# Optimization experiments

Measured on AMD Instinct MI355X. Metric: run time of the kernel, lower is better.

Reference implementation:

```python
import jax, jax.numpy as jnp
import numpy as np

K = 128      # knowledge_n (= net1 = prednet output width)
LOW = 64     # low_dim
PP = 64      # pp_dim
STU = 50000  # student_n
EXER = 20000 # exer_n
S_RANGES = [(0, 9999), (10000, 19999)]
NR = len(S_RANGES)
B = 4096


def setup_inputs() -> dict:
    key = jax.random.key(0)
    ks = jax.random.split(key, 16)

    def xavier(k, shape):
        fan_in, fan_out = shape[-1], shape[-2] if len(shape) > 1 else shape[-1]
        lim = np.sqrt(6.0 / (fan_in + fan_out))
        return jax.random.uniform(k, shape, jnp.float32, -lim, lim)

    return {
        "stu_id": jax.random.randint(ks[0], (B,), 0, STU),
        "exer_id": jax.random.randint(ks[1], (B,), 0, EXER),
        "kn_emb": jnp.ones((B, K), jnp.float32),
        "student_emb": xavier(ks[2], (NR, STU, LOW)),          # ParameterList stacked
        "prompt_stu": xavier(ks[3], (STU, PP)),
        "knowledge_emb": jax.random.normal(ks[4], (K, LOW), jnp.float32),
        "k_difficulty": xavier(ks[5], (EXER, LOW)),
        "s_exer_vectors": jax.random.uniform(ks[6], (NR, PP), jnp.float32),
        "W1": xavier(ks[7], (K, K + LOW)),                      # prednet_full1 (no bias)
        "W2": xavier(ks[8], (K, K + LOW)),                      # prednet_full2 (no bias)
        "W3": xavier(ks[9], (1, K)),                            # prednet_full3
        "b3": jnp.zeros((1,), jnp.float32),
        "fc1_W": xavier(ks[10], (K, PP + K)),
        "fc1_b": jnp.zeros((K,), jnp.float32),
        "fc2_W": xavier(ks[11], (K, PP + K)),
        "fc2_b": jnp.zeros((K,), jnp.float32),
    }


def reference(stu_id, exer_id, kn_emb, student_emb, prompt_stu, knowledge_emb,
              k_difficulty, s_exer_vectors, W1, W2, W3, b3, fc1_W, fc1_b, fc2_W, fc2_b):
    sig = jax.nn.sigmoid
    kle = knowledge_emb  # [K, LOW]

    # --- student side ---
    # prompt_stu.repeat(NR, 1) then index_select == index prompt_stu with stu_id % STU
    p_stu = prompt_stu[stu_id % STU]                              # [B, PP]
    stu_cat = student_emb.reshape(NR * STU, LOW)                  # concat of ParameterList
    old_stu = sig(stu_cat[stu_id] @ kle.T)                        # [B, K]
    stu_e = sig(jnp.concatenate([p_stu, old_stu], 1) @ fc1_W.T + fc1_b)  # [B, K]

    # --- exercise side ---
    counts = np.array([r[1] - r[0] + 1 for r in S_RANGES])
    temp_vectors = jnp.repeat(s_exer_vectors, counts, axis=0, total_repeat_length=EXER)
    p_exer = sig(temp_vectors[exer_id])                           # [B, PP]
    old_exer = sig(sig(k_difficulty[exer_id]) @ kle.T)            # [B, K]
    exer_e = sig(jnp.concatenate([p_exer, old_exer], 1) @ fc2_W.T + fc2_b)  # [B, K]

    # --- per-concept interaction ---
    # cat([x_broadcast, kn_vector], 2) @ W.T splits into x @ Wa.T + kle @ Wb.T
    W1a, W1b = W1[:, :K], W1[:, K:]
    W2a, W2b = W2[:, :K], W2[:, K:]
    preference = sig((stu_e @ W1a.T)[:, None, :] + (kle @ W1b.T)[None, :, :])   # [B, K, K]
    diff = sig((exer_e @ W2a.T)[:, None, :] + (kle @ W2b.T)[None, :, :])        # [B, K, K]

    o = sig((preference - diff) @ W3.T + b3)                      # [B, K, 1]
    sum_out = jnp.sum(o * kn_emb[:, :, None], axis=1)             # [B, 1]
    count = jnp.sum(kn_emb, axis=1, keepdims=True)
    return sum_out / count
```

## Files before the change

### kernel.cpp

```cpp
#include <hip/hip_runtime.h>
#include <hip/hip_bf16.h>

#define STUN   50000
#define BATCH  4096
#define LOG2E  1.4426950408889634f

__device__ __forceinline__ float fexp2(float x){ return __builtin_amdgcn_exp2f(x); }
__device__ __forceinline__ float frcp (float x){ return __builtin_amdgcn_rcpf(x); }
__device__ __forceinline__ float fsig (float x){ return frcp(1.0f + fexp2(-LOG2E * x)); }

__global__ __launch_bounds__(128) void k_pre(
    const float* __restrict__ kle,
    const float* __restrict__ W1,
    const float* __restrict__ W2,
    const float* __restrict__ fc1_W,
    const float* __restrict__ fc2_W,
    float* __restrict__ kleT,
    float* __restrict__ fc1T,
    float* __restrict__ fc2T,
    float* __restrict__ W1aT,
    float* __restrict__ W2aT,
    float* __restrict__ E1i,
    float* __restrict__ E2i)
{
    const int bid = blockIdx.x;
    const int t   = threadIdx.x;
    if (bid < 64) {
        const int u = bid;
        kleT[u * 128 + t] = kle[t * 64 + u];
    } else if (bid < 256) {
        const int u = bid - 64;
        fc1T[u * 128 + t] = fc1_W[t * 192 + u];
    } else if (bid < 448) {
        const int u = bid - 256;
        fc2T[u * 128 + t] = fc2_W[t * 192 + u];
    } else if (bid < 576) {
        const int u = bid - 448;
        W1aT[u * 128 + t] = W1[t * 192 + u];
    } else if (bid < 704) {
        const int u = bid - 576;
        W2aT[u * 128 + t] = W2[t * 192 + u];
    } else if (bid < 832) {
        const int j = bid - 704;
        float acc = 0.f;
        #pragma unroll
        for (int u4 = 0; u4 < 16; ++u4) {
            const float4 kv = *(const float4*)&kle[t * 64 + u4 * 4];
            const float4 wv = *(const float4*)&W1[j * 192 + 128 + u4 * 4];
            acc += kv.x * wv.x + kv.y * wv.y + kv.z * wv.z + kv.w * wv.w;
        }
        E1i[((j >> 2) * 128 + t) * 4 + (j & 3)] = fexp2(-LOG2E * acc);
    } else {
        const int j = bid - 832;
        float acc = 0.f;
        #pragma unroll
        for (int u4 = 0; u4 < 16; ++u4) {
            const float4 kv = *(const float4*)&kle[t * 64 + u4 * 4];
            const float4 wv = *(const float4*)&W2[j * 192 + 128 + u4 * 4];
            acc += kv.x * wv.x + kv.y * wv.y + kv.z * wv.z + kv.w * wv.w;
        }
        E2i[((j >> 2) * 128 + t) * 4 + (j & 3)] = fexp2(-LOG2E * acc);
    }
}

__global__ __launch_bounds__(256, 4) void k_fused(
    const int*   __restrict__ stu_id,
    const int*   __restrict__ exer_id,
    const float* __restrict__ student_emb,
    const float* __restrict__ prompt_stu,
    const float* __restrict__ k_diff,
    const float* __restrict__ s_exer,
    const float* __restrict__ kleT,
    const float* __restrict__ fc1T,
    const float* __restrict__ fc2T,
    const float* __restrict__ W1aT,
    const float* __restrict__ W2aT,
    const float* __restrict__ fc1_b,
    const float* __restrict__ fc2_b,
    const float* __restrict__ E1i,
    const float* __restrict__ E2i,
    const float* __restrict__ W3,
    const float* __restrict__ b3,
    const float* __restrict__ kn,
    float* __restrict__ out)
{
    __shared__ __align__(16) float sh_in [4][64][4];
    __shared__ __align__(16) float sh_old[2][128][4];
    __shared__ __align__(16) float sh_e  [2][128][4];
    __shared__ __align__(16) float ses   [2][4][128];
    __shared__ float r_o[4][2];
    __shared__ float r_k[4][2];

    const int t  = threadIdx.x;
    const int b0 = blockIdx.x * 4;

    {
        const int g   = t >> 6;
        const int u   = t & 63;
        const int sid = stu_id[b0 + g];
        const int eid = exer_id[b0 + g];
        const int er  = (eid >= 10000) ? 1 : 0;
        sh_in[0][u][g] = student_emb[sid * 64 + u];
        sh_in[1][u][g] = fsig(k_diff[eid * 64 + u]);
        sh_in[2][u][g] = prompt_stu[(sid % STUN) * 64 + u];
        sh_in[3][u][g] = fsig(s_exer[er * 64 + u]);
    }
    __syncthreads();

    const int w    = t >> 6;
    const int l    = t & 63;
    const int ul   = l >> 4;
    const int half = (l >> 3) & 1;
    const int iql  = l & 7;
    const int iq   = w * 8 + iql;

    float a[4][4];

#define CLR { _Pragma("unroll") for (int c = 0; c < 4; ++c) \
              _Pragma("unroll") for (int b = 0; b < 4; ++b) a[c][b] = 0.f; }

#define FMAC(c, wc) { \
    a[c][0] = fmaf(wc, x0.x, a[c][0]); a[c][1] = fmaf(wc, x0.y, a[c][1]); \
    a[c][2] = fmaf(wc, x0.z, a[c][2]); a[c][3] = fmaf(wc, x0.w, a[c][3]); }

#define GSTEP(wp, xp) { \
    const float4 w4 = *(const float4*)(wp); \
    const float4 x0 = *(const float4*)(xp); \
    FMAC(0, w4.x); FMAC(1, w4.y); FMAC(2, w4.z); FMAC(3, w4.w); }

#define COMBINE { _Pragma("unroll") for (int c = 0; c < 4; ++c) \
    _Pragma("unroll") for (int b = 0; b < 4; ++b) { \
        float v = a[c][b]; \
        v += __shfl_xor(v, 16); \
        v += __shfl_xor(v, 32); \
        a[c][b] = v; } }

    CLR;
    #pragma unroll 4
    for (int s = 0; s < 16; ++s) {
        const int u = ul + s * 4;
        GSTEP(&kleT[u * 128 + iq * 4], &sh_in[half][u][0]);
    }
    COMBINE;
    if (ul == 0) {
        #pragma unroll
        for (int c = 0; c < 4; ++c)
            *(float4*)&sh_old[half][iq * 4 + c][0] =
                make_float4(fsig(a[c][0]), fsig(a[c][1]), fsig(a[c][2]), fsig(a[c][3]));
    }
    __syncthreads();

    CLR;
    {
        const float* fcT = half ? fc2T : fc1T;
        #pragma unroll 4
        for (int s = 0; s < 16; ++s) {
            const int u = ul + s * 4;
            GSTEP(&fcT[u * 128 + iq * 4], &sh_in[2 + half][u][0]);
        }
        #pragma unroll 4
        for (int s = 0; s < 32; ++s) {
            const int u = ul + s * 4;
            GSTEP(&fcT[(64 + u) * 128 + iq * 4], &sh_old[half][u][0]);
        }
    }
    COMBINE;
    if (ul == 0) {
        const float* fcb = half ? fc2_b : fc1_b;
        #pragma unroll
        for (int c = 0; c < 4; ++c) {
            const float bias = fcb[iq * 4 + c];
            *(float4*)&sh_e[half][iq * 4 + c][0] =
                make_float4(fsig(a[c][0] + bias), fsig(a[c][1] + bias),
                            fsig(a[c][2] + bias), fsig(a[c][3] + bias));
        }
    }
    __syncthreads();

    CLR;
    {
        const float* WT = half ? W2aT : W1aT;
        #pragma unroll 4
        for (int s = 0; s < 32; ++s) {
            const int u = ul + s * 4;
            GSTEP(&WT[u * 128 + iq * 4], &sh_e[half][u][0]);
        }
    }
    COMBINE;
    if (ul == 0) {
        #pragma unroll
        for (int c = 0; c < 4; ++c) {
            #pragma unroll
            for (int b = 0; b < 4; ++b)
                ses[half][b][iq * 4 + c] = fexp2(-LOG2E * a[c][b]);
        }
    }
#undef CLR
#undef FMAC
#undef GSTEP
#undef COMBINE
    __syncthreads();

    const int k  = t & 127;
    const int bh = t >> 7;
    const int i0 = bh * 2;

    const float4* E1v = (const float4*)E1i + k;
    const float4* E2v = (const float4*)E2i + k;

    float acc0 = 0.f, acc1 = 0.f;

#define COMP(acc, esv1, esv2, e1c, e2c, w3c) { \
        const float uu = (esv1) * (e1c); \
        const float vv = (esv2) * (e2c); \
        const float dd = frcp((1.f + uu) * (1.f + vv)); \
        acc = fmaf((vv - uu) * dd, (w3c), acc); }

    #pragma unroll 4
    for (int j4 = 0; j4 < 32; ++j4) {
        const int j = j4 * 4;
        const float4 e1  = E1v[j4 * 128];
        const float4 e2  = E2v[j4 * 128];
        const float4 w3  = *(const float4*)&W3[j];
        const float4 p1a = *(const float4*)&ses[0][i0 + 0][j];
        const float4 p2a = *(const float4*)&ses[1][i0 + 0][j];
        const float4 p1b = *(const float4*)&ses[0][i0 + 1][j];
        const float4 p2b = *(const float4*)&ses[1][i0 + 1][j];
        COMP(acc0, p1a.x, p2a.x, e1.x, e2.x, w3.x);
        COMP(acc0, p1a.y, p2a.y, e1.y, e2.y, w3.y);
        COMP(acc0, p1a.z, p2a.z, e1.z, e2.z, w3.z);
        COMP(acc0, p1a.w, p2a.w, e1.w, e2.w, w3.w);
        COMP(acc1, p1b.x, p2b.x, e1.x, e2.x, w3.x);
        COMP(acc1, p1b.y, p2b.y, e1.y, e2.y, w3.y);
        COMP(acc1, p1b.z, p2b.z, e1.z, e2.z, w3.z);
        COMP(acc1, p1b.w, p2b.w, e1.w, e2.w, w3.w);
    }
#undef COMP

    const float bb3 = b3[0];
    const float o0  = fsig(acc0 + bb3);
    const float o1  = fsig(acc1 + bb3);
    const float kn0 = kn[(b0 + i0 + 0) * 128 + k];
    const float kn1 = kn[(b0 + i0 + 1) * 128 + k];
    float co0 = o0 * kn0, ck0 = kn0;
    float co1 = o1 * kn1, ck1 = kn1;
    #pragma unroll
    for (int off = 1; off < 64; off <<= 1) {
        co0 += __shfl_xor(co0, off);
        ck0 += __shfl_xor(ck0, off);
        co1 += __shfl_xor(co1, off);
        ck1 += __shfl_xor(ck1, off);
    }
    if ((t & 63) == 0) {
        r_o[w][0] = co0; r_o[w][1] = co1;
        r_k[w][0] = ck0; r_k[w][1] = ck1;
    }
    __syncthreads();
    if (t < 4) {
        const int bhh = t >> 1;
        const int i   = t & 1;
        const float so = r_o[bhh * 2][i] + r_o[bhh * 2 + 1][i];
        const float sk = r_k[bhh * 2][i] + r_k[bhh * 2 + 1][i];
        out[b0 + bhh * 2 + i] = so / sk;
    }
}

extern "C" void kernel_launch(void* const* d_in, const int* in_sizes, int n_in,
                              void* d_out, int out_size, void* d_ws, size_t ws_size,
                              hipStream_t stream)
{
    const int*   stu_id      = (const int*)  d_in[0];
    const int*   exer_id     = (const int*)  d_in[1];
    const float* kn_emb      = (const float*)d_in[2];
    const float* student_emb = (const float*)d_in[3];
    const float* prompt_stu  = (const float*)d_in[4];
    const float* kle         = (const float*)d_in[5];
    const float* k_diff      = (const float*)d_in[6];
    const float* s_exer      = (const float*)d_in[7];
    const float* W1          = (const float*)d_in[8];
    const float* W2          = (const float*)d_in[9];
    const float* W3          = (const float*)d_in[10];
    const float* b3          = (const float*)d_in[11];
    const float* fc1_W       = (const float*)d_in[12];
    const float* fc1_b       = (const float*)d_in[13];
    const float* fc2_W       = (const float*)d_in[14];
    const float* fc2_b       = (const float*)d_in[15];
    float* out = (float*)d_out;

    float* ws   = (float*)d_ws;
    float* kleT = ws;
    float* fc1T = kleT + 8192;
    float* fc2T = fc1T + 24576;
    float* W1aT = fc2T + 24576;
    float* W2aT = W1aT + 16384;
    float* E1i  = W2aT + 16384;
    float* E2i  = E1i  + 16384;

    k_pre  <<<960, 128, 0, stream>>>(kle, W1, W2, fc1_W, fc2_W,
                                     kleT, fc1T, fc2T, W1aT, W2aT, E1i, E2i);
    k_fused<<<BATCH / 4, 256, 0, stream>>>(stu_id, exer_id, student_emb, prompt_stu,
                                           k_diff, s_exer, kleT, fc1T, fc2T,
                                           W1aT, W2aT, fc1_b, fc2_b,
                                           E1i, E2i, W3, b3, kn_emb, out);
}
```

Measured before the change: 47.65 us.

## Double threads per block in fused kernel, splitting reductions across waves

Raises the fused kernel's block from 256 to 512 threads. Each GEMV stage now splits its reduction dimension across 8 lane groups, with an extra shuffle step, and the per-concept interaction loop is split in halves across wave pairs, combined through a new shared-memory buffer and barrier. The aim is more parallelism and latency hiding per batch group, at the cost of more shuffles, an extra sync, and tighter register limits from launch_bounds(512,8).

```diff
diff --git a/kernel.cpp b/kernel.cpp
--- a/kernel.cpp
+++ b/kernel.cpp
@@ -63,7 +63,7 @@
     }
 }
 
-__global__ __launch_bounds__(256, 4) void k_fused(
+__global__ __launch_bounds__(512, 8) void k_fused(
     const int*   __restrict__ stu_id,
     const int*   __restrict__ exer_id,
     const float* __restrict__ student_emb,
@@ -88,6 +88,7 @@
     __shared__ __align__(16) float sh_old[2][128][4];
     __shared__ __align__(16) float sh_e  [2][128][4];
     __shared__ __align__(16) float ses   [2][4][128];
+    __shared__ __align__(16) float red   [2][4][128];
     __shared__ float r_o[4][2];
     __shared__ float r_k[4][2];
 
@@ -95,24 +96,29 @@
     const int b0 = blockIdx.x * 4;
 
     {
-        const int g   = t >> 6;
+        const int g   = t >> 7;
+        const int sp  = (t >> 6) & 1;
         const int u   = t & 63;
         const int sid = stu_id[b0 + g];
         const int eid = exer_id[b0 + g];
-        const int er  = (eid >= 10000) ? 1 : 0;
-        sh_in[0][u][g] = student_emb[sid * 64 + u];
-        sh_in[1][u][g] = fsig(k_diff[eid * 64 + u]);
-        sh_in[2][u][g] = prompt_stu[(sid % STUN) * 64 + u];
-        sh_in[3][u][g] = fsig(s_exer[er * 64 + u]);
+        if (sp == 0) {
+            sh_in[0][u][g] = student_emb[sid * 64 + u];
+            sh_in[1][u][g] = fsig(k_diff[eid * 64 + u]);
+        } else {
+            const int er = (eid >= 10000) ? 1 : 0;
+            sh_in[2][u][g] = prompt_stu[(sid % STUN) * 64 + u];
+            sh_in[3][u][g] = fsig(s_exer[er * 64 + u]);
+        }
     }
     __syncthreads();
 
     const int w    = t >> 6;
+    const int half = w & 1;
+    const int iqo  = w >> 1;
     const int l    = t & 63;
-    const int ul   = l >> 4;
-    const int half = (l >> 3) & 1;
+    const int ul   = l >> 3;
     const int iql  = l & 7;
-    const int iq   = w * 8 + iql;
+    const int iq   = iqo * 8 + iql;
 
     float a[4][4];
 
@@ -131,14 +137,15 @@
 #define COMBINE { _Pragma("unroll") for (int c = 0; c < 4; ++c) \
     _Pragma("unroll") for (int b = 0; b < 4; ++b) { \
         float v = a[c][b]; \
+        v += __shfl_xor(v, 8); \
         v += __shfl_xor(v, 16); \
         v += __shfl_xor(v, 32); \
         a[c][b] = v; } }
 
     CLR;
     #pragma unroll 4
-    for (int s = 0; s < 16; ++s) {
-        const int u = ul + s * 4;
+    for (int s = 0; s < 8; ++s) {
+        const int u = ul + s * 8;
         GSTEP(&kleT[u * 128 + iq * 4], &sh_in[half][u][0]);
     }
     COMBINE;
@@ -154,13 +161,13 @@
     {
         const float* fcT = half ? fc2T : fc1T;
         #pragma unroll 4
+        for (int s = 0; s < 8; ++s) {
+            const int u = ul + s * 8;
+            GSTEP(&fcT[u * 128 + iq * 4], &sh_in[2 + half][u][0]);
+        }
+        #pragma unroll 4
         for (int s = 0; s < 16; ++s) {
-            const int u = ul + s * 4;
-            GSTEP(&fcT[u * 128 + iq * 4], &sh_in[2 + half][u][0]);
-        }
-        #pragma unroll 4
-        for (int s = 0; s < 32; ++s) {
-            const int u = ul + s * 4;
+            const int u = ul + s * 8;
             GSTEP(&fcT[(64 + u) * 128 + iq * 4], &sh_old[half][u][0]);
         }
     }
@@ -181,8 +188,8 @@
     {
         const float* WT = half ? W2aT : W1aT;
         #pragma unroll 4
-        for (int s = 0; s < 32; ++s) {
-            const int u = ul + s * 4;
+        for (int s = 0; s < 16; ++s) {
+            const int u = ul + s * 8;
             GSTEP(&WT[u * 128 + iq * 4], &sh_e[half][u][0]);
         }
     }
@@ -202,7 +209,9 @@
     __syncthreads();
 
     const int k  = t & 127;
-    const int bh = t >> 7;
+    const int g2 = t >> 7;
+    const int bh = g2 & 1;
+    const int jq = g2 >> 1;
     const int i0 = bh * 2;
 
     const float4* E1v = (const float4*)E1i + k;
@@ -217,8 +226,9 @@
         acc = fmaf((vv - uu) * dd, (w3c), acc); }
 
     #pragma unroll 4
-    for (int j4 = 0; j4 < 32; ++j4) {
-        const int j = j4 * 4;
+    for (int i = 0; i < 16; ++i) {
+        const int j4 = jq * 16 + i;
+        const int j  = j4 * 4;
         const float4 e1  = E1v[j4 * 128];
         const float4 e2  = E2v[j4 * 128];
         const float4 w3  = *(const float4*)&W3[j];
@@ -237,31 +247,34 @@
     }
 #undef COMP
 
-    const float bb3 = b3[0];
-    const float o0  = fsig(acc0 + bb3);
-    const float o1  = fsig(acc1 + bb3);
-    const float kn0 = kn[(b0 + i0 + 0) * 128 + k];
-    const float kn1 = kn[(b0 + i0 + 1) * 128 + k];
-    float co0 = o0 * kn0, ck0 = kn0;
-    float co1 = o1 * kn1, ck1 = kn1;
-    #pragma unroll
-    for (int off = 1; off < 64; off <<= 1) {
-        co0 += __shfl_xor(co0, off);
-        ck0 += __shfl_xor(ck0, off);
-        co1 += __shfl_xor(co1, off);
-        ck1 += __shfl_xor(ck1, off);
-    }
-    if ((t & 63) == 0) {
-        r_o[w][0] = co0; r_o[w][1] = co1;
-        r_k[w][0] = ck0; r_k[w][1] = ck1;
+    red[jq][i0 + 0][k] = acc0;
+    red[jq][i0 + 1][k] = acc1;
+    __syncthreads();
+
+    {
+        const float bb3 = b3[0];
+        const int b  = t >> 7;
+        const int kk = t & 127;
+        const float s  = red[0][b][kk] + red[1][b][kk];
+        const float o  = fsig(s + bb3);
+        const float kv = kn[(b0 + b) * 128 + kk];
+        float co = o * kv, ck = kv;
+        #pragma unroll
+        for (int off = 1; off < 64; off <<= 1) {
+            co += __shfl_xor(co, off);
+            ck += __shfl_xor(ck, off);
+        }
+        if ((t & 63) == 0) {
+            const int kh = w & 1;
+            r_o[b][kh] = co;
+            r_k[b][kh] = ck;
+        }
     }
     __syncthreads();
     if (t < 4) {
-        const int bhh = t >> 1;
-        const int i   = t & 1;
-        const float so = r_o[bhh * 2][i] + r_o[bhh * 2 + 1][i];
-        const float sk = r_k[bhh * 2][i] + r_k[bhh * 2 + 1][i];
-        out[b0 + bhh * 2 + i] = so / sk;
+        const float so = r_o[t][0] + r_o[t][1];
+        const float sk = r_k[t][0] + r_k[t][1];
+        out[b0 + t] = so / sk;
     }
 }
 
@@ -298,7 +311,7 @@
 
     k_pre  <<<960, 128, 0, stream>>>(kle, W1, W2, fc1_W, fc2_W,
                                      kleT, fc1T, fc2T, W1aT, W2aT, E1i, E2i);
-    k_fused<<<BATCH / 4, 256, 0, stream>>>(stu_id, exer_id, student_emb, prompt_stu,
+    k_fused<<<BATCH / 4, 512, 0, stream>>>(stu_id, exer_id, student_emb, prompt_stu,
                                            k_diff, s_exer, kleT, fc1T, fc2T,
                                            W1aT, W2aT, fc1_b, fc2_b,
                                            E1i, E2i, W3, b3, kn_emb, out);
```

After: 84.58 us. 77.5% more time.
